# Optimization experiments

Measured on AMD Instinct MI355X. Metric: run time of the kernel, lower is better.

Reference implementation:

```python
import jax, jax.numpy as jnp
import numpy as np

SRC_LEN, TGT_LEN, BATCH = 256, 128, 256
NH, NE, NSYM = 512, 256, 64


def setup_inputs() -> dict:
    key = jax.random.key(0)
    ks = jax.random.split(key, 14)
    w = lambda k, shape: jax.random.normal(k, shape, jnp.float32) * 0.05
    return {
        "src_enc": jax.random.normal(ks[0], (SRC_LEN, BATCH, NH), jnp.float32),
        "tgt": jax.random.randint(ks[1], (TGT_LEN, BATCH, 1), 0, NSYM, jnp.int32),
        "src_lengths": jax.random.randint(ks[2], (BATCH,), 1, SRC_LEN + 1, jnp.int32),
        "emb_table": w(ks[3], (NSYM, NE)),
        "Ws_w": w(ks[4], (NH, NH)), "Ws_b": jnp.zeros((NH,), jnp.float32),
        "Wz_w": w(ks[5], (NH, NE + 2 * NH)), "Wz_b": jnp.zeros((NH,), jnp.float32),
        "Wr_w": w(ks[6], (NH, NE + 2 * NH)), "Wr_b": jnp.zeros((NH,), jnp.float32),
        "Wn_w": w(ks[7], (NH, NE + 2 * NH)), "Wn_b": jnp.zeros((NH,), jnp.float32),
        "Wa_w": w(ks[8], (NH, 2 * NH)), "Wa_b": jnp.zeros((NH,), jnp.float32),
        "va_w": w(ks[9], (1, NH)),
        "Wo_w": w(ks[10], (NH, NE + 2 * NH)), "Wo_b": jnp.zeros((NH,), jnp.float32),
    }


def reference(src_enc, tgt, src_lengths, emb_table,
              Ws_w, Ws_b, Wz_w, Wz_b, Wr_w, Wr_b, Wn_w, Wn_b,
              Wa_w, Wa_b, va_w, Wo_w, Wo_b):
    src_len, batch, nh = src_enc.shape
    # src_mask: [src_len, batch] True where position < length
    mask = jnp.arange(src_len)[:, None] < src_lengths[None, :]
    tgt_embed = emb_table[tgt[..., 0]]                     # [T, B, E]
    s0 = jnp.tanh(src_enc[0] @ Ws_w.T + Ws_b)              # [B, H]
    # Split Wa into the s-part and src_enc-part; encoder projection is
    # loop-invariant, compute it once (same math as cat+Linear).
    Wa_s, Wa_e = Wa_w[:, :nh], Wa_w[:, nh:]
    enc_proj = jnp.einsum('sbh,gh->sbg', src_enc, Wa_e) + Wa_b  # [S, B, H]
    va = va_w[0]                                           # [H]
    neg_inf = jnp.float32(-jnp.inf)

    def step(s, emb_i):
        h = jnp.tanh(enc_proj + s @ Wa_s.T)                # [S, B, H]
        ei = jnp.einsum('sbh,h->sb', h, va)                # [S, B]
        ei = jnp.where(mask, ei, neg_inf)
        ai = jax.nn.softmax(ei, axis=0)                    # [S, B]
        ci = jnp.einsum('sb,sbh->bh', ai, src_enc)         # [B, H]
        x = jnp.concatenate([emb_i, s, ci], axis=-1)       # [B, E+2H]
        ti = x @ Wo_w.T + Wo_b
        zi = jax.nn.sigmoid(x @ Wz_w.T + Wz_b)
        ri = jax.nn.sigmoid(x @ Wr_w.T + Wr_b)
        xn = jnp.concatenate([emb_i, ri * s, ci], axis=-1)
        ni = jnp.tanh(xn @ Wn_w.T + Wn_b)
        s_new = (1.0 - zi) * s + zi * ni
        return s_new, (ti, s, ai.T)

    _, (dec_outputs, dec_states, dec_attns) = jax.lax.scan(step, s0, tgt_embed[:-1])
    # dec_outputs/dec_states: [T-1, B, H]; dec_attns: [T-1, B, S]
    return dec_outputs, dec_states, dec_attns
```

## Files before the change

kernel.cpp:

```cpp
#include <hip/hip_runtime.h>
#include <hip/hip_bf16.h>
#include <cstdint>
#include <cstddef>

namespace {

constexpr int S_LEN  = 256;
constexpr int BATCH  = 256;
constexpr int NH     = 512;
constexpr int NE     = 256;
constexpr int NSTEPS = 127;
constexpr int N1     = 2048;
constexpr size_t SB        = (size_t)S_LEN * BATCH;
constexpr size_t SRC_ELEMS = SB * NH;

typedef __attribute__((ext_vector_type(8))) short  short8v;
typedef __attribute__((ext_vector_type(4))) float  float4v;
typedef unsigned short us;

constexpr int EPI_F32 = 0, EPI_EPROJ = 1, EPI_STEP1 = 2, EPI_STEP2 = 3, EPI_S0 = 4;

__device__ __forceinline__ float bf2f(us u) {
  union { unsigned int i; float f; } c; c.i = ((unsigned int)u) << 16; return c.f;
}
__device__ __forceinline__ us f2bf(float f) {
  union { float f; unsigned int i; } c; c.f = f;
  unsigned int x = c.i;
  return (us)((x + 0x7FFFu + ((x >> 16) & 1u)) >> 16);
}
__device__ __forceinline__ float tanh2(float x) {
  return 1.f - 2.f * __builtin_amdgcn_rcpf(__expf(2.f * x) + 1.f);
}
__device__ __forceinline__ float sigm(float x) {
  return __builtin_amdgcn_rcpf(1.f + __expf(-x));
}


__global__ void k_conv_src(const float* __restrict__ src, us* __restrict__ dst) {
  size_t i = (size_t)blockIdx.x * blockDim.x + threadIdx.x;
  size_t stride = (size_t)gridDim.x * blockDim.x;
  for (size_t j = i * 4; j < SRC_ELEMS; j += stride * 4) {
    float4 v = *(const float4*)(src + j);
    dst[j+0] = f2bf(v.x); dst[j+1] = f2bf(v.y);
    dst[j+2] = f2bf(v.z); dst[j+3] = f2bf(v.w);
  }
}

__global__ void k_conv_w(const float* __restrict__ Wo, const float* __restrict__ Wz,
                         const float* __restrict__ Wr, const float* __restrict__ Wn,
                         const float* __restrict__ Wa, const float* __restrict__ Ws,
                         const float* __restrict__ Wob, const float* __restrict__ Wzb,
                         const float* __restrict__ Wrb, const float* __restrict__ Wnb,
                         us* __restrict__ W1cat, us* __restrict__ Wns,
                         us* __restrict__ Was, us* __restrict__ Wae,
                         us* __restrict__ Wsbf, float* __restrict__ bcat) {
  const int T1 = 2048 * 1280;
  const int T2 = 512 * 512;
  const int total = T1 + 4 * T2 + 2048;
  int i = blockIdx.x * blockDim.x + threadIdx.x;
  int stride = gridDim.x * blockDim.x;
  for (; i < total; i += stride) {
    int idx = i;
    if (idx < T1) {
      int row = idx / 1280, col = idx - row * 1280;
      float v;
      if      (row < 512)  v = Wo[row * 1280 + col];
      else if (row < 1024) v = Wz[(row - 512) * 1280 + col];
      else if (row < 1536) v = Wr[(row - 1024) * 1280 + col];
      else {
        int g = row - 1536;
        v = (col >= 256 && col < 768) ? 0.f : Wn[g * 1280 + col];
      }
      W1cat[idx] = f2bf(v);
    } else if ((idx -= T1) < T2) {
      int g = idx >> 9, j = idx & 511;
      Wns[idx] = f2bf(Wn[g * 1280 + 256 + j]);
    } else if ((idx -= T2) < T2) {
      int g = idx >> 9, h = idx & 511;
      Was[idx] = f2bf(Wa[g * 1024 + h]);
    } else if ((idx -= T2) < T2) {
      int g = idx >> 9, h = idx & 511;
      Wae[idx] = f2bf(Wa[g * 1024 + 512 + h]);
    } else if ((idx -= T2) < T2) {
      Wsbf[idx] = f2bf(Ws[idx]);
    } else {
      idx -= T2;
      bcat[idx] = (idx < 512) ? Wob[idx]
                : (idx < 1024) ? Wzb[idx - 512]
                : (idx < 1536) ? Wrb[idx - 1024]
                               : Wnb[idx - 1536];
    }
  }
}

__global__ void k_emb(const int* __restrict__ tgt, const float* __restrict__ table,
                      us* __restrict__ emb) {
  const int total = NSTEPS * BATCH * NE;
  int i = blockIdx.x * blockDim.x + threadIdx.x;
  int stride = gridDim.x * blockDim.x;
  for (; i < total; i += stride) {
    int e  = i & (NE - 1);
    int tb = i >> 8;
    int sym = tgt[tb];
    emb[i] = f2bf(table[sym * NE + e]);
  }
}

template<int EPI>
__global__ __launch_bounds__(256) void k_g64(
    const us* __restrict__ A0, const us* __restrict__ A1, const us* __restrict__ A2,
    const us* __restrict__ Bw, int K,
    const float* __restrict__ bias,
    float* __restrict__ f0, float* __restrict__ f1, float* __restrict__ f2,
    us* __restrict__ g0,
    const float* __restrict__ sf) {
  constexpr bool X3 = (EPI == EPI_STEP1);
  __shared__ us As[2][4096];
  __shared__ us Bs[2][4096];
  const int tid = threadIdx.x;
  const int m0 = blockIdx.x * 64, n0 = blockIdx.y * 64;
  const int srow  = tid >> 2;
  const int c0    = (tid & 3) * 16;
  const int cbyte = c0 * 2;
  const int nit   = K >> 6;
  short8v ar0, ar1, br0, br1;

  auto loadA = [&](int k0) {
    const int cc0 = k0 + c0, cc1 = cc0 + 8;
    if (X3) {
      const us* p0 = (cc0 < 256) ? A0 + (size_t)(m0 + srow) * 256 + cc0
                   : (cc0 < 768) ? A1 + (size_t)(m0 + srow) * 512 + (cc0 - 256)
                                 : A2 + (size_t)(m0 + srow) * 512 + (cc0 - 768);
      const us* p1 = (cc1 < 256) ? A0 + (size_t)(m0 + srow) * 256 + cc1
                   : (cc1 < 768) ? A1 + (size_t)(m0 + srow) * 512 + (cc1 - 256)
                                 : A2 + (size_t)(m0 + srow) * 512 + (cc1 - 768);
      ar0 = *(const short8v*)p0;
      ar1 = *(const short8v*)p1;
    } else {
      const us* p = A0 + (size_t)(m0 + srow) * K + cc0;
      ar0 = *(const short8v*)p;
      ar1 = *(const short8v*)(p + 8);
    }
    const us* q = Bw + (size_t)(n0 + srow) * K + cc0;
    br0 = *(const short8v*)q;
    br1 = *(const short8v*)(q + 8);
  };
  auto stage = [&](int buf) {
    char* ab = (char*)As + buf * 8192;
    char* bb = (char*)Bs + buf * 8192;
    const int sw = (srow & 7) << 4;
    const int o0 = srow * 128 + (cbyte ^ sw);
    const int o1 = srow * 128 + ((cbyte + 16) ^ sw);
    *(short8v*)(ab + o0) = ar0;
    *(short8v*)(ab + o1) = ar1;
    *(short8v*)(bb + o0) = br0;
    *(short8v*)(bb + o1) = br1;
  };

  const int lane = tid & 63, wave = tid >> 6;
  const int wm = (wave >> 1) * 32, wn = (wave & 1) * 32;
  const int fr = lane & 15, kq = lane >> 4;
  const int ra0 = wm + fr, ra1 = wm + 16 + fr;
  const int rb0 = wn + fr, rb1 = wn + 16 + fr;
  float4v acc00 = {0,0,0,0}, acc01 = {0,0,0,0}, acc10 = {0,0,0,0}, acc11 = {0,0,0,0};

  loadA(0);
  stage(0);
  for (int it = 0; it < nit; ++it) {
    __syncthreads();
    if (it + 1 < nit) loadA((it + 1) << 6);
    const char* ab = (const char*)As + (it & 1) * 8192;
    const char* bb = (const char*)Bs + (it & 1) * 8192;
    #pragma unroll
    for (int ks = 0; ks < 2; ++ks) {
      const int cb2 = ks * 64 + kq * 16;
      short8v a0 = *(const short8v*)(ab + ra0 * 128 + (cb2 ^ ((ra0 & 7) << 4)));
      short8v a1 = *(const short8v*)(ab + ra1 * 128 + (cb2 ^ ((ra1 & 7) << 4)));
      short8v b0 = *(const short8v*)(bb + rb0 * 128 + (cb2 ^ ((rb0 & 7) << 4)));
      short8v b1 = *(const short8v*)(bb + rb1 * 128 + (cb2 ^ ((rb1 & 7) << 4)));
      acc00 = __builtin_amdgcn_mfma_f32_16x16x32_bf16(a0, b0, acc00, 0, 0, 0);
      acc01 = __builtin_amdgcn_mfma_f32_16x16x32_bf16(a0, b1, acc01, 0, 0, 0);
      acc10 = __builtin_amdgcn_mfma_f32_16x16x32_bf16(a1, b0, acc10, 0, 0, 0);
      acc11 = __builtin_amdgcn_mfma_f32_16x16x32_bf16(a1, b1, acc11, 0, 0, 0);
    }
    if (it + 1 < nit) stage((it + 1) & 1);
  }

  #pragma unroll
  for (int am = 0; am < 2; ++am) {
    #pragma unroll
    for (int bn = 0; bn < 2; ++bn) {
      float4v a = am ? (bn ? acc11 : acc10) : (bn ? acc01 : acc00);
      #pragma unroll
      for (int r = 0; r < 4; ++r) {
        const int rowO = m0 + wm + am * 16 + kq * 4 + r;
        const int colO = n0 + wn + bn * 16 + fr;
        float v = a[r];
        if (EPI == EPI_F32) {
          f0[(size_t)rowO * 512 + colO] = v;
        } else if (EPI == EPI_S0) {
          float tv = tanh2(v + bias[colO]);
          f0[(size_t)rowO * 512 + colO] = tv;
          g0[(size_t)rowO * 512 + colO] = f2bf(tv);
        } else if (EPI == EPI_EPROJ) {
          g0[(size_t)rowO * 512 + colO] = f2bf(v + bias[colO]);
        } else if (EPI == EPI_STEP1) {
          v += bias[colO];
          const int q = colO >> 9, j = colO & 511;
          const size_t idx = (size_t)rowO * 512 + j;
          if      (q == 0) f0[idx] = v;
          else if (q == 1) f1[idx] = sigm(v);
          else if (q == 2) g0[idx] = f2bf(sigm(v) * sf[idx]);
          else             f2[idx] = v;
        } else {
          const size_t idx = (size_t)rowO * 512 + colO;
          float nv = tanh2(v + f2[idx]);
          float z  = bias[idx];
          float so = f1[idx];
          float sn = (1.f - z) * so + z * nv;
          f0[idx] = so;
          f1[idx] = sn;
          g0[idx] = f2bf(sn);
        }
      }
    }
  }
}

__global__ __launch_bounds__(512) void k_attn(
    const us* __restrict__ ep,
    const us* __restrict__ srcb,
    const float* __restrict__ sWa,
    const float* __restrict__ va,
    const int* __restrict__ slen,
    float* __restrict__ attn_out,
    us* __restrict__ ci_bf) {
  __shared__ float ei[S_LEN];
  __shared__ float ai[S_LEN];
  __shared__ float red[8];
  const int b = blockIdx.x, tid = threadIdx.x;
  const int lane = tid & 63, wave = tid >> 6;
  const int g0 = lane * 8;
  float qv[8], vv[8];
  {
    const float* qp = sWa + b * NH + g0;
    const float* vp = va + g0;
    #pragma unroll
    for (int j = 0; j < 8; j++) { qv[j] = qp[j]; vv[j] = vp[j]; }
  }
  const int len = slen[b];

  for (int s = wave; s < S_LEN; s += 8) {
    short8v v = *(const short8v*)(ep + ((size_t)s * BATCH + b) * NH + g0);
    float acc = 0.f;
    #pragma unroll
    for (int j = 0; j < 8; j++)
      acc += tanh2(bf2f((us)v[j]) + qv[j]) * vv[j];
    #pragma unroll
    for (int off = 32; off > 0; off >>= 1) acc += __shfl_xor(acc, off, 64);
    if (lane == 0) ei[s] = (s < len) ? acc : -3.0e38f;
  }
  __syncthreads();

  float e = (tid < S_LEN) ? ei[tid] : -3.0e38f;
  float m = e;
  #pragma unroll
  for (int off = 32; off > 0; off >>= 1) m = fmaxf(m, __shfl_xor(m, off, 64));
  if (lane == 0) red[wave] = m;
  __syncthreads();
  m = red[0];
  #pragma unroll
  for (int w = 1; w < 8; w++) m = fmaxf(m, red[w]);
  float p = (tid < S_LEN) ? __expf(e - m) : 0.f;
  float sum = p;
  #pragma unroll
  for (int off = 32; off > 0; off >>= 1) sum += __shfl_xor(sum, off, 64);
  __syncthreads();
  if (lane == 0) red[wave] = sum;
  __syncthreads();
  float tot = red[0];
  #pragma unroll
  for (int w = 1; w < 8; w++) tot += red[w];
  float inv = __builtin_amdgcn_rcpf(tot);
  if (tid < S_LEN) {
    float a = p * inv;
    ai[tid] = a;
    attn_out[(size_t)b * S_LEN + tid] = a;
  }
  __syncthreads();

  float acc = 0.f;
  const us* sp = srcb + (size_t)b * NH + tid;
  #pragma unroll 8
  for (int s = 0; s < S_LEN; s++) acc += ai[s] * bf2f(sp[(size_t)s * BATCH * NH]);
  ci_bf[b * NH + tid] = f2bf(acc);
}

}

extern "C" void kernel_launch(void* const* d_in, const int* in_sizes, int n_in,
                              void* d_out, int out_size, void* d_ws, size_t ws_size,
                              hipStream_t stream) {
  const float* src_enc  = (const float*)d_in[0];
  const int*   tgt      = (const int*)d_in[1];
  const int*   slen     = (const int*)d_in[2];
  const float* emb_tab  = (const float*)d_in[3];
  const float* Wsw      = (const float*)d_in[4];
  const float* Wsb      = (const float*)d_in[5];
  const float* Wzw      = (const float*)d_in[6];
  const float* Wzb      = (const float*)d_in[7];
  const float* Wrw      = (const float*)d_in[8];
  const float* Wrb      = (const float*)d_in[9];
  const float* Wnw      = (const float*)d_in[10];
  const float* Wnb      = (const float*)d_in[11];
  const float* Waw      = (const float*)d_in[12];
  const float* Wab      = (const float*)d_in[13];
  const float* vaw      = (const float*)d_in[14];
  const float* Wow      = (const float*)d_in[15];
  const float* Wob      = (const float*)d_in[16];

  char* ws = (char*)d_ws;
  size_t off = 0;
  auto alloc = [&](size_t bytes) -> void* {
    void* p = ws + off;
    off = (off + bytes + 255) & ~(size_t)255;
    return p;
  };
  us*    src_bf = (us*)alloc(SRC_ELEMS * 2);
  us*    ep     = (us*)alloc(SRC_ELEMS * 2);
  us*    emb_bf = (us*)alloc((size_t)NSTEPS * BATCH * NE * 2);
  us*    W1cat  = (us*)alloc((size_t)N1 * 1280 * 2);
  us*    Wns    = (us*)alloc((size_t)512 * 512 * 2);
  us*    Was    = (us*)alloc((size_t)512 * 512 * 2);
  us*    Wae    = (us*)alloc((size_t)512 * 512 * 2);
  us*    Wsbf   = (us*)alloc((size_t)512 * 512 * 2);
  float* bcat   = (float*)alloc((size_t)N1 * 4);
  float* s_f32  = (float*)alloc((size_t)BATCH * NH * 4);
  us*    s_bf   = (us*)alloc((size_t)BATCH * NH * 2);
  float* sWa    = (float*)alloc((size_t)BATCH * NH * 4);
  float* zi     = (float*)alloc((size_t)BATCH * NH * 4);
  float* npart  = (float*)alloc((size_t)BATCH * NH * 4);
  us*    xn_bf  = (us*)alloc((size_t)BATCH * NH * 2);
  us*    ci_bf  = (us*)alloc((size_t)BATCH * NH * 2);

  float* out         = (float*)d_out;
  float* dec_outputs = out;
  float* dec_states  = out + (size_t)NSTEPS * BATCH * NH;
  float* dec_attns   = dec_states + (size_t)NSTEPS * BATCH * NH;

  k_conv_src<<<4096, 256, 0, stream>>>(src_enc, src_bf);
  k_conv_w<<<2048, 256, 0, stream>>>(Wow, Wzw, Wrw, Wnw, Waw, Wsw,
                                     Wob, Wzb, Wrb, Wnb,
                                     W1cat, Wns, Was, Wae, Wsbf, bcat);
  k_emb<<<2048, 256, 0, stream>>>(tgt, emb_tab, emb_bf);
  k_g64<EPI_S0><<<dim3(4, 8), 256, 0, stream>>>(
      src_bf, nullptr, nullptr, Wsbf, 512, Wsb, s_f32, nullptr, nullptr, s_bf, nullptr);
  k_g64<EPI_EPROJ><<<dim3(1024, 8), 256, 0, stream>>>(
      src_bf, nullptr, nullptr, Wae, 512, Wab, nullptr, nullptr, nullptr, ep, nullptr);

  for (int t = 0; t < NSTEPS; t++) {
    k_g64<EPI_F32><<<dim3(4, 8), 256, 0, stream>>>(
        s_bf, nullptr, nullptr, Was, 512, nullptr, sWa, nullptr, nullptr, nullptr, nullptr);
    k_attn<<<BATCH, 512, 0, stream>>>(ep, src_bf, sWa, vaw, slen,
                                      dec_attns + (size_t)t * BATCH * S_LEN, ci_bf);
    k_g64<EPI_STEP1><<<dim3(4, 32), 256, 0, stream>>>(
        emb_bf + (size_t)t * BATCH * NE, s_bf, ci_bf, W1cat, 1280, bcat,
        dec_outputs + (size_t)t * BATCH * NH, zi, npart, xn_bf, s_f32);
    k_g64<EPI_STEP2><<<dim3(4, 8), 256, 0, stream>>>(
        xn_bf, nullptr, nullptr, Wns, 512, zi,
        dec_states + (size_t)t * BATCH * NH, s_f32, npart, s_bf, nullptr);
  }
}
```

Measured before the change: 9.611 ms.

## Fuse decoder time loop into a persistent cooperative kernel with grid syncs

The per-step chain of four kernel launches (127 steps) becomes one cooperative persistent kernel that runs every stage of every step and separates the stages with grid-wide barriers. The source encoding and its projection are stored batch-major so each attention block reads contiguous rows. The context reduction is vectorised across waves, and the tanh in the score is rewritten algebraically to save operations. The GEMM tiles are widened to 64x128 with 512 threads. The aim is to remove launch overhead and improve memory access, at the cost of leaving most blocks idle during the small GEMM phases and paying four grid syncs per step.

```diff
diff --git a/kernel.cpp b/kernel.cpp
--- a/kernel.cpp
+++ b/kernel.cpp
@@ -1,7 +1,10 @@
 #include <hip/hip_runtime.h>
+#include <hip/hip_cooperative_groups.h>
 #include <hip/hip_bf16.h>
 #include <cstdint>
 #include <cstddef>
+
+namespace cg = cooperative_groups;
 
 namespace {
 
@@ -37,12 +40,17 @@
 
 
 __global__ void k_conv_src(const float* __restrict__ src, us* __restrict__ dst) {
-  size_t i = (size_t)blockIdx.x * blockDim.x + threadIdx.x;
-  size_t stride = (size_t)gridDim.x * blockDim.x;
-  for (size_t j = i * 4; j < SRC_ELEMS; j += stride * 4) {
-    float4 v = *(const float4*)(src + j);
-    dst[j+0] = f2bf(v.x); dst[j+1] = f2bf(v.y);
-    dst[j+2] = f2bf(v.z); dst[j+3] = f2bf(v.w);
+  const int total = S_LEN * BATCH * 64;
+  int i = blockIdx.x * blockDim.x + threadIdx.x;
+  int stride = gridDim.x * blockDim.x;
+  for (; i < total; i += stride) {
+    int c = i & 63, s = (i >> 6) & 255, b = i >> 14;
+    const float* p = src + ((size_t)s * BATCH + b) * NH + c * 8;
+    float4 v0 = *(const float4*)p;
+    float4 v1 = *(const float4*)(p + 4);
+    us o[8] = { f2bf(v0.x), f2bf(v0.y), f2bf(v0.z), f2bf(v0.w),
+                f2bf(v1.x), f2bf(v1.y), f2bf(v1.z), f2bf(v1.w) };
+    *(short8v*)(dst + (size_t)i * 8) = *(const short8v*)o;
   }
 }
 
@@ -107,77 +115,63 @@
 }
 
 template<int EPI>
-__global__ __launch_bounds__(256) void k_g64(
+__device__ __forceinline__ void gemm_tile(
+    char* smem, int m0, int n0,
     const us* __restrict__ A0, const us* __restrict__ A1, const us* __restrict__ A2,
-    const us* __restrict__ Bw, int K,
-    const float* __restrict__ bias,
-    float* __restrict__ f0, float* __restrict__ f1, float* __restrict__ f2,
-    us* __restrict__ g0,
-    const float* __restrict__ sf) {
-  constexpr bool X3 = (EPI == EPI_STEP1);
-  __shared__ us As[2][4096];
-  __shared__ us Bs[2][4096];
+    int lda, const us* __restrict__ Bw, int ldb, int K,
+    const float* __restrict__ bias, float* __restrict__ f0, float* __restrict__ f1,
+    float* __restrict__ f2, us* __restrict__ g0, const float* __restrict__ sf) {
   const int tid = threadIdx.x;
-  const int m0 = blockIdx.x * 64, n0 = blockIdx.y * 64;
-  const int srow  = tid >> 2;
-  const int c0    = (tid & 3) * 16;
-  const int cbyte = c0 * 2;
-  const int nit   = K >> 6;
-  short8v ar0, ar1, br0, br1;
-
-  auto loadA = [&](int k0) {
-    const int cc0 = k0 + c0, cc1 = cc0 + 8;
-    if (X3) {
-      const us* p0 = (cc0 < 256) ? A0 + (size_t)(m0 + srow) * 256 + cc0
-                   : (cc0 < 768) ? A1 + (size_t)(m0 + srow) * 512 + (cc0 - 256)
-                                 : A2 + (size_t)(m0 + srow) * 512 + (cc0 - 768);
-      const us* p1 = (cc1 < 256) ? A0 + (size_t)(m0 + srow) * 256 + cc1
-                   : (cc1 < 768) ? A1 + (size_t)(m0 + srow) * 512 + (cc1 - 256)
-                                 : A2 + (size_t)(m0 + srow) * 512 + (cc1 - 768);
-      ar0 = *(const short8v*)p0;
-      ar1 = *(const short8v*)p1;
+  char* As0 = smem;
+  char* Bs0 = smem + 16384;
+  const int arow = tid >> 3, ac = (tid & 7) * 8;
+  const int brow = tid >> 2, bc = (tid & 3) * 16;
+  short8v ar, br0, br1;
+
+  auto loadT = [&](int k0) {
+    if (EPI == EPI_STEP1) {
+      const int cc = k0 + ac;
+      const us* p = (cc < 256) ? A0 + (size_t)(m0 + arow) * 256 + cc
+                  : (cc < 768) ? A1 + (size_t)(m0 + arow) * 512 + (cc - 256)
+                               : A2 + (size_t)(m0 + arow) * 512 + (cc - 768);
+      ar = *(const short8v*)p;
     } else {
-      const us* p = A0 + (size_t)(m0 + srow) * K + cc0;
-      ar0 = *(const short8v*)p;
-      ar1 = *(const short8v*)(p + 8);
-    }
-    const us* q = Bw + (size_t)(n0 + srow) * K + cc0;
+      ar = *(const short8v*)(A0 + (size_t)(m0 + arow) * lda + (k0 + ac));
+    }
+    const us* q = Bw + (size_t)(n0 + brow) * ldb + (k0 + bc);
     br0 = *(const short8v*)q;
     br1 = *(const short8v*)(q + 8);
   };
   auto stage = [&](int buf) {
-    char* ab = (char*)As + buf * 8192;
-    char* bb = (char*)Bs + buf * 8192;
-    const int sw = (srow & 7) << 4;
-    const int o0 = srow * 128 + (cbyte ^ sw);
-    const int o1 = srow * 128 + ((cbyte + 16) ^ sw);
-    *(short8v*)(ab + o0) = ar0;
-    *(short8v*)(ab + o1) = ar1;
-    *(short8v*)(bb + o0) = br0;
-    *(short8v*)(bb + o1) = br1;
+    *(short8v*)(As0 + buf * 8192 + arow * 128 + ((ac * 2) ^ ((arow & 7) << 4))) = ar;
+    char* bb = Bs0 + buf * 16384 + brow * 128;
+    const int sw = (brow & 7) << 4;
+    *(short8v*)(bb + ((bc * 2) ^ sw)) = br0;
+    *(short8v*)(bb + ((bc * 2 + 16) ^ sw)) = br1;
   };
 
   const int lane = tid & 63, wave = tid >> 6;
-  const int wm = (wave >> 1) * 32, wn = (wave & 1) * 32;
+  const int wm = (wave >> 2) * 32, wn = (wave & 3) * 32;
   const int fr = lane & 15, kq = lane >> 4;
-  const int ra0 = wm + fr, ra1 = wm + 16 + fr;
-  const int rb0 = wn + fr, rb1 = wn + 16 + fr;
+  const int ra0 = wm + fr, ra1 = ra0 + 16;
+  const int rb0 = wn + fr, rb1 = rb0 + 16;
   float4v acc00 = {0,0,0,0}, acc01 = {0,0,0,0}, acc10 = {0,0,0,0}, acc11 = {0,0,0,0};
 
-  loadA(0);
+  loadT(0);
   stage(0);
+  const int nit = K >> 6;
   for (int it = 0; it < nit; ++it) {
     __syncthreads();
-    if (it + 1 < nit) loadA((it + 1) << 6);
-    const char* ab = (const char*)As + (it & 1) * 8192;
-    const char* bb = (const char*)Bs + (it & 1) * 8192;
+    if (it + 1 < nit) loadT((it + 1) << 6);
+    const char* ab = As0 + (it & 1) * 8192;
+    const char* bb = Bs0 + (it & 1) * 16384;
     #pragma unroll
     for (int ks = 0; ks < 2; ++ks) {
-      const int cb2 = ks * 64 + kq * 16;
-      short8v a0 = *(const short8v*)(ab + ra0 * 128 + (cb2 ^ ((ra0 & 7) << 4)));
-      short8v a1 = *(const short8v*)(ab + ra1 * 128 + (cb2 ^ ((ra1 & 7) << 4)));
-      short8v b0 = *(const short8v*)(bb + rb0 * 128 + (cb2 ^ ((rb0 & 7) << 4)));
-      short8v b1 = *(const short8v*)(bb + rb1 * 128 + (cb2 ^ ((rb1 & 7) << 4)));
+      const int cb = ks * 64 + kq * 16;
+      short8v a0 = *(const short8v*)(ab + ra0 * 128 + (cb ^ ((ra0 & 7) << 4)));
+      short8v a1 = *(const short8v*)(ab + ra1 * 128 + (cb ^ ((ra1 & 7) << 4)));
+      short8v b0 = *(const short8v*)(bb + rb0 * 128 + (cb ^ ((rb0 & 7) << 4)));
+      short8v b1 = *(const short8v*)(bb + rb1 * 128 + (cb ^ ((rb1 & 7) << 4)));
       acc00 = __builtin_amdgcn_mfma_f32_16x16x32_bf16(a0, b0, acc00, 0, 0, 0);
       acc01 = __builtin_amdgcn_mfma_f32_16x16x32_bf16(a0, b1, acc01, 0, 0, 0);
       acc10 = __builtin_amdgcn_mfma_f32_16x16x32_bf16(a1, b0, acc10, 0, 0, 0);
@@ -227,73 +221,141 @@
   }
 }
 
-__global__ __launch_bounds__(512) void k_attn(
-    const us* __restrict__ ep,
-    const us* __restrict__ srcb,
-    const float* __restrict__ sWa,
-    const float* __restrict__ va,
-    const int* __restrict__ slen,
-    float* __restrict__ attn_out,
-    us* __restrict__ ci_bf) {
-  __shared__ float ei[S_LEN];
-  __shared__ float ai[S_LEN];
-  __shared__ float red[8];
-  const int b = blockIdx.x, tid = threadIdx.x;
-  const int lane = tid & 63, wave = tid >> 6;
-  const int g0 = lane * 8;
-  float qv[8], vv[8];
+template<int EPI>
+__global__ __launch_bounds__(512, 2) void k_gemm(
+    const us* __restrict__ A0, int lda, const us* __restrict__ Bw, int ldb, int K,
+    const float* __restrict__ bias, float* __restrict__ f0, us* __restrict__ g0) {
+  __shared__ alignas(16) char smem[49152];
+  gemm_tile<EPI>(smem, blockIdx.x * 64, blockIdx.y * 128,
+                 A0, nullptr, nullptr, lda, Bw, ldb, K,
+                 bias, f0, nullptr, nullptr, g0, nullptr);
+}
+
+struct KArgs {
+  const us* src_t; const us* ep_t; const us* emb_bf;
+  const us* W1cat; const us* Wns; const us* Was;
+  const float* bcat; const float* vaw; const int* slen;
+  us* s_bf; float* s_f32; float* sWa; float* zi; float* npart;
+  us* xn_bf; us* ci_bf;
+  float* dec_outputs; float* dec_states; float* dec_attns;
+};
+
+__global__ __launch_bounds__(512, 2) void k_steps(KArgs a) {
+  __shared__ alignas(16) char smem[49152];
+  cg::grid_group grid = cg::this_grid();
+  const int blk = blockIdx.x, tid = threadIdx.x;
+  const int lane = tid & 63, wave = tid >> 6, g0l = lane * 8;
+  const int b = blk;
+  const int len = a.slen[b];
+
+  float vv2[8]; float sumv = 0.f;
   {
-    const float* qp = sWa + b * NH + g0;
-    const float* vp = va + g0;
+    const float* vp = a.vaw + g0l;
     #pragma unroll
-    for (int j = 0; j < 8; j++) { qv[j] = qp[j]; vv[j] = vp[j]; }
-  }
-  const int len = slen[b];
-
-  for (int s = wave; s < S_LEN; s += 8) {
-    short8v v = *(const short8v*)(ep + ((size_t)s * BATCH + b) * NH + g0);
-    float acc = 0.f;
+    for (int j = 0; j < 8; j++) { vv2[j] = 2.f * vp[j]; sumv += vp[j]; }
     #pragma unroll
-    for (int j = 0; j < 8; j++)
-      acc += tanh2(bf2f((us)v[j]) + qv[j]) * vv[j];
-    #pragma unroll
-    for (int off = 32; off > 0; off >>= 1) acc += __shfl_xor(acc, off, 64);
-    if (lane == 0) ei[s] = (s < len) ? acc : -3.0e38f;
-  }
-  __syncthreads();
-
-  float e = (tid < S_LEN) ? ei[tid] : -3.0e38f;
-  float m = e;
-  #pragma unroll
-  for (int off = 32; off > 0; off >>= 1) m = fmaxf(m, __shfl_xor(m, off, 64));
-  if (lane == 0) red[wave] = m;
-  __syncthreads();
-  m = red[0];
-  #pragma unroll
-  for (int w = 1; w < 8; w++) m = fmaxf(m, red[w]);
-  float p = (tid < S_LEN) ? __expf(e - m) : 0.f;
-  float sum = p;
-  #pragma unroll
-  for (int off = 32; off > 0; off >>= 1) sum += __shfl_xor(sum, off, 64);
-  __syncthreads();
-  if (lane == 0) red[wave] = sum;
-  __syncthreads();
-  float tot = red[0];
-  #pragma unroll
-  for (int w = 1; w < 8; w++) tot += red[w];
-  float inv = __builtin_amdgcn_rcpf(tot);
-  if (tid < S_LEN) {
-    float a = p * inv;
-    ai[tid] = a;
-    attn_out[(size_t)b * S_LEN + tid] = a;
-  }
-  __syncthreads();
-
-  float acc = 0.f;
-  const us* sp = srcb + (size_t)b * NH + tid;
-  #pragma unroll 8
-  for (int s = 0; s < S_LEN; s++) acc += ai[s] * bf2f(sp[(size_t)s * BATCH * NH]);
-  ci_bf[b * NH + tid] = f2bf(acc);
+    for (int off = 32; off > 0; off >>= 1) sumv += __shfl_xor(sumv, off, 64);
+  }
+
+  for (int t = 0; t < NSTEPS; ++t) {
+    if (blk < 16) {
+      gemm_tile<EPI_F32>(smem, (blk >> 2) * 64, (blk & 3) * 128,
+                         a.s_bf, nullptr, nullptr, 512, a.Was, 512, 512,
+                         nullptr, a.sWa, nullptr, nullptr, nullptr, nullptr);
+    }
+    grid.sync();
+
+    {
+      float* ei   = (float*)smem;
+      float* ai   = ei + 256;
+      float* red  = ai + 256;
+      float* red8 = (float*)(smem + 4096);
+
+      float q2[8];
+      {
+        const float* qp = a.sWa + b * NH + g0l;
+        #pragma unroll
+        for (int j = 0; j < 8; j++) q2[j] = 2.f * qp[j];
+      }
+      const us* epb = a.ep_t + ((size_t)b * S_LEN + wave) * NH + g0l;
+      for (int s = wave; s < S_LEN; s += 8, epb += 8 * NH) {
+        short8v v = *(const short8v*)epb;
+        float acc = 0.f;
+        #pragma unroll
+        for (int j = 0; j < 8; j++) {
+          float arg = __builtin_fmaf(bf2f((us)v[j]), 2.f, q2[j]);
+          acc = __builtin_fmaf(vv2[j],
+                __builtin_amdgcn_rcpf(__expf(arg) + 1.f), acc);
+        }
+        #pragma unroll
+        for (int off = 32; off > 0; off >>= 1) acc += __shfl_xor(acc, off, 64);
+        if (lane == 0) ei[s] = (s < len) ? (sumv - acc) : -3.0e38f;
+      }
+      __syncthreads();
+
+      float e = (tid < S_LEN) ? ei[tid] : -3.0e38f;
+      float m = e;
+      #pragma unroll
+      for (int off = 32; off > 0; off >>= 1) m = fmaxf(m, __shfl_xor(m, off, 64));
+      if (lane == 0) red[wave] = m;
+      __syncthreads();
+      m = red[0];
+      #pragma unroll
+      for (int w = 1; w < 8; w++) m = fmaxf(m, red[w]);
+      float p = (tid < S_LEN) ? __expf(e - m) : 0.f;
+      float sum = p;
+      #pragma unroll
+      for (int off = 32; off > 0; off >>= 1) sum += __shfl_xor(sum, off, 64);
+      __syncthreads();
+      if (lane == 0) red[wave] = sum;
+      __syncthreads();
+      float tot = red[0];
+      #pragma unroll
+      for (int w = 1; w < 8; w++) tot += red[w];
+      float inv = __builtin_amdgcn_rcpf(tot);
+      if (tid < S_LEN) {
+        float av = p * inv;
+        ai[tid] = av;
+        a.dec_attns[((size_t)t * BATCH + b) * S_LEN + tid] = av;
+      }
+      __syncthreads();
+
+      float acc8[8] = {0,0,0,0,0,0,0,0};
+      const us* sb = a.src_t + ((size_t)b * S_LEN + wave) * NH + g0l;
+      for (int s = wave; s < S_LEN; s += 8, sb += 8 * NH) {
+        short8v v = *(const short8v*)sb;
+        float av = ai[s];
+        #pragma unroll
+        for (int j = 0; j < 8; j++)
+          acc8[j] = __builtin_fmaf(av, bf2f((us)v[j]), acc8[j]);
+      }
+      #pragma unroll
+      for (int j = 0; j < 8; j++) red8[wave * NH + g0l + j] = acc8[j];
+      __syncthreads();
+      float cv = 0.f;
+      #pragma unroll
+      for (int w = 0; w < 8; w++) cv += red8[w * NH + tid];
+      a.ci_bf[b * NH + tid] = f2bf(cv);
+    }
+    grid.sync();
+
+    if (blk < 64) {
+      gemm_tile<EPI_STEP1>(smem, (blk >> 4) * 64, (blk & 15) * 128,
+                           a.emb_bf + (size_t)t * BATCH * NE, a.s_bf, a.ci_bf, 0,
+                           a.W1cat, 1280, 1280,
+                           a.bcat, a.dec_outputs + (size_t)t * BATCH * NH,
+                           a.zi, a.npart, a.xn_bf, a.s_f32);
+    }
+    grid.sync();
+
+    if (blk < 16) {
+      gemm_tile<EPI_STEP2>(smem, (blk >> 2) * 64, (blk & 3) * 128,
+                           a.xn_bf, nullptr, nullptr, 512, a.Wns, 512, 512,
+                           a.zi, a.dec_states + (size_t)t * BATCH * NH,
+                           a.s_f32, a.npart, a.s_bf, nullptr);
+    }
+    grid.sync();
+  }
 }
 
 }
@@ -326,8 +388,8 @@
     off = (off + bytes + 255) & ~(size_t)255;
     return p;
   };
-  us*    src_bf = (us*)alloc(SRC_ELEMS * 2);
-  us*    ep     = (us*)alloc(SRC_ELEMS * 2);
+  us*    src_t  = (us*)alloc(SRC_ELEMS * 2);
+  us*    ep_t   = (us*)alloc(SRC_ELEMS * 2);
   us*    emb_bf = (us*)alloc((size_t)NSTEPS * BATCH * NE * 2);
   us*    W1cat  = (us*)alloc((size_t)N1 * 1280 * 2);
   us*    Wns    = (us*)alloc((size_t)512 * 512 * 2);
@@ -348,26 +410,24 @@
   float* dec_states  = out + (size_t)NSTEPS * BATCH * NH;
   float* dec_attns   = dec_states + (size_t)NSTEPS * BATCH * NH;
 
-  k_conv_src<<<4096, 256, 0, stream>>>(src_enc, src_bf);
+  k_conv_src<<<4096, 256, 0, stream>>>(src_enc, src_t);
   k_conv_w<<<2048, 256, 0, stream>>>(Wow, Wzw, Wrw, Wnw, Waw, Wsw,
                                      Wob, Wzb, Wrb, Wnb,
                                      W1cat, Wns, Was, Wae, Wsbf, bcat);
   k_emb<<<2048, 256, 0, stream>>>(tgt, emb_tab, emb_bf);
-  k_g64<EPI_S0><<<dim3(4, 8), 256, 0, stream>>>(
-      src_bf, nullptr, nullptr, Wsbf, 512, Wsb, s_f32, nullptr, nullptr, s_bf, nullptr);
-  k_g64<EPI_EPROJ><<<dim3(1024, 8), 256, 0, stream>>>(
-      src_bf, nullptr, nullptr, Wae, 512, Wab, nullptr, nullptr, nullptr, ep, nullptr);
-
-  for (int t = 0; t < NSTEPS; t++) {
-    k_g64<EPI_F32><<<dim3(4, 8), 256, 0, stream>>>(
-        s_bf, nullptr, nullptr, Was, 512, nullptr, sWa, nullptr, nullptr, nullptr, nullptr);
-    k_attn<<<BATCH, 512, 0, stream>>>(ep, src_bf, sWa, vaw, slen,
-                                      dec_attns + (size_t)t * BATCH * S_LEN, ci_bf);
-    k_g64<EPI_STEP1><<<dim3(4, 32), 256, 0, stream>>>(
-        emb_bf + (size_t)t * BATCH * NE, s_bf, ci_bf, W1cat, 1280, bcat,
-        dec_outputs + (size_t)t * BATCH * NH, zi, npart, xn_bf, s_f32);
-    k_g64<EPI_STEP2><<<dim3(4, 8), 256, 0, stream>>>(
-        xn_bf, nullptr, nullptr, Wns, 512, zi,
-        dec_states + (size_t)t * BATCH * NH, s_f32, npart, s_bf, nullptr);
-  }
-}
+  k_gemm<EPI_S0><<<dim3(4, 4), 512, 0, stream>>>(
+      src_t, S_LEN * NH, Wsbf, 512, 512, Wsb, s_f32, s_bf);
+  k_gemm<EPI_EPROJ><<<dim3(1024, 4), 512, 0, stream>>>(
+      src_t, 512, Wae, 512, 512, Wab, nullptr, ep_t);
+
+  KArgs a;
+  a.src_t = src_t; a.ep_t = ep_t; a.emb_bf = emb_bf;
+  a.W1cat = W1cat; a.Wns = Wns; a.Was = Was;
+  a.bcat = bcat; a.vaw = vaw; a.slen = slen;
+  a.s_bf = s_bf; a.s_f32 = s_f32; a.sWa = sWa; a.zi = zi; a.npart = npart;
+  a.xn_bf = xn_bf; a.ci_bf = ci_bf;
+  a.dec_outputs = dec_outputs; a.dec_states = dec_states; a.dec_attns = dec_attns;
+  void* kargs[] = { &a };
+  hipLaunchCooperativeKernel((const void*)k_steps, dim3(256), dim3(512),
+                             kargs, 0, stream);
+}
```

Result: slower. 22.88 ms (+138.1%).
